# Performance work log

Hardware: AMD Instinct MI355X
Metric: run time of the kernel (lower is better)

Reference implementation:

```python
import jax, jax.numpy as jnp
import numpy as np
import math

N_HEADS = 16

def setup_inputs() -> dict:
    key = jax.random.key(0)
    k1, k2, k3 = jax.random.split(key, 3)
    B, S, D = 2, 2048, 1024
    x = jax.random.normal(k1, (B, S, D), dtype=jnp.float32)
    qkv = 0.01 * jax.random.normal(k2, (3 * D, D), dtype=jnp.float32)
    wo = 0.01 * jax.random.normal(k3, (D, D), dtype=jnp.float32)
    return {"x": x, "qkv": qkv, "wo": wo}

def reference(x, qkv, wo):
    B, S, D = x.shape
    H = N_HEADS
    dh = D // H
    QKV = x @ qkv.T                      # [B,S,3D]
    Q, K, V = jnp.split(QKV, 3, axis=-1)
    q = Q.reshape(B, S, H, dh).transpose(0, 2, 1, 3)  # [B,H,S,dh]
    k = K.reshape(B, S, H, dh).transpose(0, 2, 1, 3)
    v = V.reshape(B, S, H, dh).transpose(0, 2, 1, 3)
    scores = jnp.einsum('bhqd,bhkd->bhqk', q, k) / math.sqrt(float(dh))
    # Faithful to original: multiply by lower-triangular mask, then set
    # exact zeros to -inf (masked positions become 0 then -inf).
    mask = jnp.tril(jnp.ones((S, S), dtype=scores.dtype))
    scores = scores * mask[None, None, :, :]
    scores = jnp.where(scores == 0, -jnp.inf, scores)
    attn = jax.nn.softmax(scores, axis=-1)
    out = jnp.einsum('bhqk,bhkd->bhqd', attn, v)       # [B,H,S,dh]
    out = out.transpose(0, 2, 1, 3).reshape(B, S, D)
    return out @ wo.T
```

## Files before the change

### kernel.cpp

```cpp
#include <hip/hip_runtime.h>

typedef unsigned short u16;
typedef unsigned int u32;
typedef __bf16 bf16x8 __attribute__((ext_vector_type(8)));
typedef float f32x4 __attribute__((ext_vector_type(4)));
typedef u16 u16x4 __attribute__((ext_vector_type(4)));

#define GL2LDS16(g, l)                                                         \
    __builtin_amdgcn_global_load_lds(                                          \
        (__attribute__((address_space(1))) const void*)(g),                    \
        (__attribute__((address_space(3))) void*)(l), 16, 0, 0)

#define SYNC_VM(n) asm volatile("s_waitcnt vmcnt(" #n ")\ns_barrier" ::: "memory")
#define BAR()      asm volatile("s_barrier" ::: "memory")

__device__ __forceinline__ u16 f2bf(float f) {
    union { float f; u32 u; } x; x.f = f;
    u32 r = x.u + 0x7FFFu + ((x.u >> 16) & 1u);
    return (u16)(r >> 16);
}

__device__ __forceinline__ u32 pack2bf(float f0, float f1) {
    union { float f; u32 u; } a, b;
    a.f = f0; b.f = f1;
    return __builtin_amdgcn_perm(b.u + 0x8000u, a.u + 0x8000u, 0x07060302u);
}

__device__ __forceinline__ bf16x8 scale_frag(bf16x8 v) {
#pragma unroll
    for (int i = 0; i < 8; ++i) v[i] = (__bf16)((float)v[i] * 0.1803368801f);
    return v;
}

__global__ __launch_bounds__(256) void convert_all_kernel(const float* __restrict__ x,
                                                          const float* __restrict__ qkv,
                                                          const float* __restrict__ wo,
                                                          u16* __restrict__ out) {
    int i = (blockIdx.x * 256 + threadIdx.x) * 4;
    const float* src;
    int off;
    if (i < 4194304)      { src = x;   off = i; }
    else if (i < 7340032) { src = qkv; off = i - 4194304; }
    else                  { src = wo;  off = i - 7340032; }
    float4 v = *(const float4*)(src + off);
    u16x4 o;
    o.x = f2bf(v.x); o.y = f2bf(v.y); o.z = f2bf(v.z); o.w = f2bf(v.w);
    *(u16x4*)(out + i) = o;
}

template <int TM, bool OUT_BF16>
__global__ __launch_bounds__(256) void gemm_bt(const u16* __restrict__ A,
                                               const u16* __restrict__ B,
                                               void* __restrict__ Cout,
                                               int M, int N, int K) {
    constexpr int MI = TM / 32;
    __shared__ u16 As[2][TM * 32];
    __shared__ u16 Bs[2][128 * 32];
    const int tid = threadIdx.x;
    const int w = tid >> 6, lane = tid & 63, ln = lane & 15, qd = lane >> 4;
    const int wr = w >> 1, wc = w & 1;
    const int m0 = blockIdx.y * TM, n0 = blockIdx.x * 128;

    const int srow = tid >> 2, scol = (tid & 3) * 8;
    const u16* Abase = A + (size_t)(m0 + srow) * K + scol;
    const u16* Bbase = B + (size_t)(n0 + srow) * K + scol;

    f32x4 acc[MI][4] = {};
    const int nsteps = K >> 5;

#pragma unroll
    for (int it = 0; it < TM / 64; ++it)
        GL2LDS16(Abase + (size_t)(it * 64) * K, &As[0][(tid + it * 256) * 8]);
#pragma unroll
    for (int it = 0; it < 2; ++it)
        GL2LDS16(Bbase + (size_t)(it * 64) * K, &Bs[0][(tid + it * 256) * 8]);

    for (int s = 0; s < nsteps; ++s) {
        const u16* Ab = As[s & 1];
        const u16* Bb = Bs[s & 1];
        if (s + 1 < nsteps) {
            const int nk = (s + 1) << 5;
            const int nb = (s + 1) & 1;
#pragma unroll
            for (int it = 0; it < TM / 64; ++it)
                GL2LDS16(Abase + (size_t)(it * 64) * K + nk, &As[nb][(tid + it * 256) * 8]);
#pragma unroll
            for (int it = 0; it < 2; ++it)
                GL2LDS16(Bbase + (size_t)(it * 64) * K + nk, &Bs[nb][(tid + it * 256) * 8]);
            if constexpr (TM == 128) SYNC_VM(4); else SYNC_VM(3);
        } else {
            SYNC_VM(0);
        }

        bf16x8 af[MI], bfr[4];
#pragma unroll
        for (int i = 0; i < MI; ++i)
            af[i] = *(const bf16x8*)&Ab[(wr * (TM / 2) + i * 16 + ln) * 32 + qd * 8];
#pragma unroll
        for (int j = 0; j < 4; ++j)
            bfr[j] = *(const bf16x8*)&Bb[(wc * 64 + j * 16 + ln) * 32 + qd * 8];
#pragma unroll
        for (int i = 0; i < MI; ++i)
#pragma unroll
            for (int j = 0; j < 4; ++j)
                acc[i][j] = __builtin_amdgcn_mfma_f32_16x16x32_bf16(af[i], bfr[j], acc[i][j], 0, 0, 0);
        BAR();
    }

#pragma unroll
    for (int i = 0; i < MI; ++i)
#pragma unroll
        for (int j = 0; j < 4; ++j)
#pragma unroll
            for (int r = 0; r < 4; ++r) {
                int row = m0 + wr * (TM / 2) + i * 16 + qd * 4 + r;
                int col = n0 + wc * 64 + j * 16 + ln;
                float v = acc[i][j][r];
                if constexpr (OUT_BF16)
                    ((u16*)Cout)[(size_t)row * N + col] = f2bf(v);
                else
                    ((float*)Cout)[(size_t)row * N + col] = v;
            }
}

__global__ __launch_bounds__(256) void vtrans_kernel(const u16* __restrict__ QKV,
                                                     u16* __restrict__ VtG) {
    __shared__ u16 T[64 * 72];
    const int tid = threadIdx.x;
    const int bh = blockIdx.y;
    const int b = bh >> 4, h = bh & 15;
    const int s0 = blockIdx.x * 64;
#pragma unroll
    for (int it = 0; it < 2; ++it) {
        int idx = it * 256 + tid;
        int sl = idx >> 3, dg = (idx & 7) << 3;
        union { uint4 v; u16 u[8]; } raw;
        raw.v = *(const uint4*)(QKV + (size_t)(b * 2048 + s0 + sl) * 3072 + 2048 + h * 64 + dg);
#pragma unroll
        for (int j = 0; j < 8; ++j) T[(dg + j) * 72 + sl] = raw.u[j];
    }
    __syncthreads();
#pragma unroll
    for (int it = 0; it < 2; ++it) {
        int idx = it * 256 + tid;
        int d = idx >> 3, sg = (idx & 7) << 3;
        *(uint4*)(VtG + ((size_t)(bh * 64 + d)) * 2048 + s0 + sg) = *(uint4*)&T[d * 72 + sg];
    }
}

__global__ __launch_bounds__(128) void attn_kernel(const u16* __restrict__ QKV,
                                                   const u16* __restrict__ VtG,
                                                   u16* __restrict__ AO) {
    __shared__ u16 Ks[2][64 * 64];
    __shared__ u16 Vts[2][64 * 64];
    __shared__ u16 Pls[2][16 * 64];

    const int tid = threadIdx.x;
    const int w = tid >> 6, lane = tid & 63, ln = lane & 15, qd = lane >> 4;
    const int b = blockIdx.z, h = blockIdx.y;
    const int qtA = blockIdx.x;
    const int qtB = 63 - qtA;
    const int XA = qtA * 32 + w * 16;
    const int XB = qtB * 32 + w * 16;
    const int myqA = XA + ln, myqB = XB + ln;
    const int bh = b * 16 + h;
    const int swz = ln & 7;
    const int nch = (qtB >> 1) + 1;

    const int sr0 = tid >> 3;
    const int sg = (tid & 7) ^ (sr0 & 7);
    const u16* ksrc = QKV + (size_t)(b * 2048 + sr0) * 3072 + 1024 + h * 64 + sg * 8;
    const u16* vsrc = VtG + (size_t)(bh * 64 + sr0) * 2048 + sg * 8;

#pragma unroll
    for (int i = 0; i < 4; ++i) {
        GL2LDS16(ksrc + (size_t)(i * 16) * 3072, &Ks[0][(i * 128 + tid) * 8]);
        GL2LDS16(vsrc + (size_t)(i * 16) * 2048, &Vts[0][(i * 128 + tid) * 8]);
    }

    const u16* qpA = QKV + (size_t)(b * 2048 + myqA) * 3072 + h * 64;
    const u16* qpB = QKV + (size_t)(b * 2048 + myqB) * 3072 + h * 64;
    bf16x8 qfA0 = scale_frag(*(const bf16x8*)(qpA + qd * 8));
    bf16x8 qfA1 = scale_frag(*(const bf16x8*)(qpA + 32 + qd * 8));
    bf16x8 qfB0 = scale_frag(*(const bf16x8*)(qpB + qd * 8));
    bf16x8 qfB1 = scale_frag(*(const bf16x8*)(qpB + 32 + qd * 8));

    f32x4 oA[4] = {}, oB[4] = {};
    float lA = 0.f, lB = 0.f;
    u16* Pw = Pls[w];

    for (int c = 0; c < nch; ++c) {
        if (c + 1 < nch) {
            const int k1 = (c + 1) * 64;
            const int nb = (c + 1) & 1;
#pragma unroll
            for (int i = 0; i < 4; ++i) {
                GL2LDS16(ksrc + (size_t)(k1 + i * 16) * 3072, &Ks[nb][(i * 128 + tid) * 8]);
                GL2LDS16(vsrc + (size_t)(i * 16) * 2048 + k1, &Vts[nb][(i * 128 + tid) * 8]);
            }
            SYNC_VM(8);
        } else {
            SYNC_VM(0);
        }
        const u16* Kb = Ks[c & 1];
        const u16* Vb = Vts[c & 1];
        const bool actA = (c * 64 <= XA + 15);

        f32x4 sA[4], sB[4];
#pragma unroll
        for (int kt = 0; kt < 4; ++kt) {
            const u16* kr = Kb + (kt * 16 + ln) * 64;
            bf16x8 kf0 = *(const bf16x8*)(kr + ((qd ^ swz) * 8));
            bf16x8 kf1 = *(const bf16x8*)(kr + (((qd + 4) ^ swz) * 8));
            f32x4 z = {0.f, 0.f, 0.f, 0.f};
            z = __builtin_amdgcn_mfma_f32_16x16x32_bf16(kf0, qfB0, z, 0, 0, 0);
            z = __builtin_amdgcn_mfma_f32_16x16x32_bf16(kf1, qfB1, z, 0, 0, 0);
            sB[kt] = z;
            if (actA) {
                f32x4 y = {0.f, 0.f, 0.f, 0.f};
                y = __builtin_amdgcn_mfma_f32_16x16x32_bf16(kf0, qfA0, y, 0, 0, 0);
                y = __builtin_amdgcn_mfma_f32_16x16x32_bf16(kf1, qfA1, y, 0, 0, 0);
                sA[kt] = y;
            }
        }

        if (c * 64 + 63 > XB) {
#pragma unroll
            for (int kt = 0; kt < 4; ++kt)
#pragma unroll
                for (int r = 0; r < 4; ++r) {
                    int key = c * 64 + kt * 16 + qd * 4 + r;
                    if (key > myqB) sB[kt][r] = -1e30f;
                }
        }
#pragma unroll
        for (int kt = 0; kt < 4; ++kt) {
            float p0 = exp2f(sB[kt][0]), p1 = exp2f(sB[kt][1]);
            float p2 = exp2f(sB[kt][2]), p3 = exp2f(sB[kt][3]);
            lB += (p0 + p1) + (p2 + p3);
            uint2 pk = {pack2bf(p0, p1), pack2bf(p2, p3)};
            int g = kt * 2 + (qd >> 1);
            *(uint2*)&Pw[ln * 64 + ((g ^ swz) * 8) + (qd & 1) * 4] = pk;
        }
        bf16x8 pfB0 = *(const bf16x8*)&Pw[ln * 64 + ((qd ^ swz) * 8)];
        bf16x8 pfB1 = *(const bf16x8*)&Pw[ln * 64 + (((qd + 4) ^ swz) * 8)];

        bf16x8 pfA0, pfA1;
        if (actA) {
            if (c * 64 + 63 > XA) {
#pragma unroll
                for (int kt = 0; kt < 4; ++kt)
#pragma unroll
                    for (int r = 0; r < 4; ++r) {
                        int key = c * 64 + kt * 16 + qd * 4 + r;
                        if (key > myqA) sA[kt][r] = -1e30f;
                    }
            }
#pragma unroll
            for (int kt = 0; kt < 4; ++kt) {
                float p0 = exp2f(sA[kt][0]), p1 = exp2f(sA[kt][1]);
                float p2 = exp2f(sA[kt][2]), p3 = exp2f(sA[kt][3]);
                lA += (p0 + p1) + (p2 + p3);
                uint2 pk = {pack2bf(p0, p1), pack2bf(p2, p3)};
                int g = kt * 2 + (qd >> 1);
                *(uint2*)&Pw[ln * 64 + ((g ^ swz) * 8) + (qd & 1) * 4] = pk;
            }
            pfA0 = *(const bf16x8*)&Pw[ln * 64 + ((qd ^ swz) * 8)];
            pfA1 = *(const bf16x8*)&Pw[ln * 64 + (((qd + 4) ^ swz) * 8)];
        }

#pragma unroll
        for (int dt = 0; dt < 4; ++dt) {
            const u16* vr = Vb + (dt * 16 + ln) * 64;
            bf16x8 vf0 = *(const bf16x8*)(vr + ((qd ^ swz) * 8));
            bf16x8 vf1 = *(const bf16x8*)(vr + (((qd + 4) ^ swz) * 8));
            oB[dt] = __builtin_amdgcn_mfma_f32_16x16x32_bf16(vf0, pfB0, oB[dt], 0, 0, 0);
            oB[dt] = __builtin_amdgcn_mfma_f32_16x16x32_bf16(vf1, pfB1, oB[dt], 0, 0, 0);
            if (actA) {
                oA[dt] = __builtin_amdgcn_mfma_f32_16x16x32_bf16(vf0, pfA0, oA[dt], 0, 0, 0);
                oA[dt] = __builtin_amdgcn_mfma_f32_16x16x32_bf16(vf1, pfA1, oA[dt], 0, 0, 0);
            }
        }
        BAR();
    }

    lA += __shfl_xor(lA, 16); lA += __shfl_xor(lA, 32);
    lB += __shfl_xor(lB, 16); lB += __shfl_xor(lB, 32);
    float invA = 1.0f / lA, invB = 1.0f / lB;
#pragma unroll
    for (int dt = 0; dt < 4; ++dt) {
        uint2 ovA = {pack2bf(oA[dt][0] * invA, oA[dt][1] * invA),
                     pack2bf(oA[dt][2] * invA, oA[dt][3] * invA)};
        *(uint2*)&AO[(size_t)(b * 2048 + myqA) * 1024 + h * 64 + dt * 16 + qd * 4] = ovA;
        uint2 ovB = {pack2bf(oB[dt][0] * invB, oB[dt][1] * invB),
                     pack2bf(oB[dt][2] * invB, oB[dt][3] * invB)};
        *(uint2*)&AO[(size_t)(b * 2048 + myqB) * 1024 + h * 64 + dt * 16 + qd * 4] = ovB;
    }
}

extern "C" void kernel_launch(void* const* d_in, const int* in_sizes, int n_in,
                              void* d_out, int out_size, void* d_ws, size_t ws_size,
                              hipStream_t stream) {
    const float* x   = (const float*)d_in[0];
    const float* qkv = (const float*)d_in[1];
    const float* wo  = (const float*)d_in[2];
    float* out = (float*)d_out;

    char* ws = (char*)d_ws;
    u16* xb   = (u16*)(ws + 0);
    u16* qkvb = (u16*)(ws + 8388608);
    u16* wob  = (u16*)(ws + 14680064);
    u16* QKVo = (u16*)(ws + 16777216);
    u16* AO   = (u16*)(ws + 41943040);
    u16* VtG  = (u16*)(ws + 0);

    convert_all_kernel<<<8192, 256, 0, stream>>>(x, qkv, wo, xb);

    gemm_bt<128, true><<<dim3(24, 32), 256, 0, stream>>>(xb, qkvb, QKVo, 4096, 3072, 1024);

    vtrans_kernel<<<dim3(32, 32), 256, 0, stream>>>(QKVo, VtG);

    attn_kernel<<<dim3(32, 16, 2), 128, 0, stream>>>(QKVo, VtG, AO);

    gemm_bt<64, false><<<dim3(8, 64), 256, 0, stream>>>(AO, wob, out, 4096, 1024, 1024);
}
```

Before: 202.7 us.

## Split attention key range across two blocks and merge partials in normalize pass

```diff
diff --git a/kernel.cpp b/kernel.cpp
--- a/kernel.cpp
+++ b/kernel.cpp
@@ -24,6 +24,10 @@
     union { float f; u32 u; } a, b;
     a.f = f0; b.f = f1;
     return __builtin_amdgcn_perm(b.u + 0x8000u, a.u + 0x8000u, 0x07060302u);
+}
+
+__device__ __forceinline__ float bits2f(u32 u) {
+    union { u32 u; float f; } x; x.u = u; return x.f;
 }
 
 __device__ __forceinline__ bf16x8 scale_frag(bf16x8 v) {
@@ -148,35 +152,35 @@
     }
 }
 
-__global__ __launch_bounds__(128) void attn_kernel(const u16* __restrict__ QKV,
+__global__ __launch_bounds__(256) void attn_kernel(u16* __restrict__ QKV,
                                                    const u16* __restrict__ VtG,
-                                                   u16* __restrict__ AO) {
+                                                   u16* __restrict__ AO,
+                                                   float* __restrict__ Lp) {
     __shared__ u16 Ks[2][64 * 64];
     __shared__ u16 Vts[2][64 * 64];
-    __shared__ u16 Pls[2][16 * 64];
+    __shared__ u16 Pls[4][16 * 64];
 
     const int tid = threadIdx.x;
     const int w = tid >> 6, lane = tid & 63, ln = lane & 15, qd = lane >> 4;
     const int b = blockIdx.z, h = blockIdx.y;
-    const int qtA = blockIdx.x;
-    const int qtB = 63 - qtA;
-    const int XA = qtA * 32 + w * 16;
-    const int XB = qtB * 32 + w * 16;
+    const int pair = blockIdx.x >> 1;
+    const int k = blockIdx.x & 1;
+    const int qtA = pair, qtB = 31 - pair;
+    const int XA = qtA * 64 + w * 16, XB = qtB * 64 + w * 16;
     const int myqA = XA + ln, myqB = XB + ln;
     const int bh = b * 16 + h;
     const int swz = ln & 7;
-    const int nch = (qtB >> 1) + 1;
+    const int nch = qtB + 1;
 
     const int sr0 = tid >> 3;
     const int sg = (tid & 7) ^ (sr0 & 7);
     const u16* ksrc = QKV + (size_t)(b * 2048 + sr0) * 3072 + 1024 + h * 64 + sg * 8;
     const u16* vsrc = VtG + (size_t)(bh * 64 + sr0) * 2048 + sg * 8;
 
-#pragma unroll
-    for (int i = 0; i < 4; ++i) {
-        GL2LDS16(ksrc + (size_t)(i * 16) * 3072, &Ks[0][(i * 128 + tid) * 8]);
-        GL2LDS16(vsrc + (size_t)(i * 16) * 2048, &Vts[0][(i * 128 + tid) * 8]);
-    }
+    GL2LDS16(ksrc + (size_t)(k * 64) * 3072, &Ks[0][tid * 8]);
+    GL2LDS16(ksrc + (size_t)(k * 64 + 32) * 3072, &Ks[0][tid * 8 + 2048]);
+    GL2LDS16(vsrc + k * 64, &Vts[0][tid * 8]);
+    GL2LDS16(vsrc + k * 64 + 32 * 2048, &Vts[0][tid * 8 + 2048]);
 
     const u16* qpA = QKV + (size_t)(b * 2048 + myqA) * 3072 + h * 64;
     const u16* qpB = QKV + (size_t)(b * 2048 + myqB) * 3072 + h * 64;
@@ -189,21 +193,22 @@
     float lA = 0.f, lB = 0.f;
     u16* Pw = Pls[w];
 
-    for (int c = 0; c < nch; ++c) {
-        if (c + 1 < nch) {
-            const int k1 = (c + 1) * 64;
-            const int nb = (c + 1) & 1;
-#pragma unroll
-            for (int i = 0; i < 4; ++i) {
-                GL2LDS16(ksrc + (size_t)(k1 + i * 16) * 3072, &Ks[nb][(i * 128 + tid) * 8]);
-                GL2LDS16(vsrc + (size_t)(i * 16) * 2048 + k1, &Vts[nb][(i * 128 + tid) * 8]);
-            }
-            SYNC_VM(8);
+    for (int c = k; c < nch; c += 2) {
+        const int j = (c - k) >> 1;
+        const int buf = j & 1;
+        if (c + 2 < nch) {
+            const int k1 = (c + 2) * 64;
+            const int nb = buf ^ 1;
+            GL2LDS16(ksrc + (size_t)k1 * 3072, &Ks[nb][tid * 8]);
+            GL2LDS16(ksrc + (size_t)(k1 + 32) * 3072, &Ks[nb][tid * 8 + 2048]);
+            GL2LDS16(vsrc + k1, &Vts[nb][tid * 8]);
+            GL2LDS16(vsrc + k1 + 32 * 2048, &Vts[nb][tid * 8 + 2048]);
+            SYNC_VM(4);
         } else {
             SYNC_VM(0);
         }
-        const u16* Kb = Ks[c & 1];
-        const u16* Vb = Vts[c & 1];
+        const u16* Kb = Ks[buf];
+        const u16* Vb = Vts[buf];
         const bool actA = (c * 64 <= XA + 15);
 
         f32x4 sA[4], sB[4];
@@ -286,16 +291,44 @@
 
     lA += __shfl_xor(lA, 16); lA += __shfl_xor(lA, 32);
     lB += __shfl_xor(lB, 16); lB += __shfl_xor(lB, 32);
-    float invA = 1.0f / lA, invB = 1.0f / lB;
+    u16* Op = k ? (QKV + 2048) : AO;
+    const size_t ost = k ? 3072 : 1024;
+    if (qd == 0) {
+        Lp[(size_t)k * 65536 + (size_t)(b * 2048 + myqA) * 16 + h] = lA;
+        Lp[(size_t)k * 65536 + (size_t)(b * 2048 + myqB) * 16 + h] = lB;
+    }
 #pragma unroll
     for (int dt = 0; dt < 4; ++dt) {
-        uint2 ovA = {pack2bf(oA[dt][0] * invA, oA[dt][1] * invA),
-                     pack2bf(oA[dt][2] * invA, oA[dt][3] * invA)};
-        *(uint2*)&AO[(size_t)(b * 2048 + myqA) * 1024 + h * 64 + dt * 16 + qd * 4] = ovA;
-        uint2 ovB = {pack2bf(oB[dt][0] * invB, oB[dt][1] * invB),
-                     pack2bf(oB[dt][2] * invB, oB[dt][3] * invB)};
-        *(uint2*)&AO[(size_t)(b * 2048 + myqB) * 1024 + h * 64 + dt * 16 + qd * 4] = ovB;
-    }
+        uint2 ovA = {pack2bf(oA[dt][0], oA[dt][1]), pack2bf(oA[dt][2], oA[dt][3])};
+        *(uint2*)&Op[(size_t)(b * 2048 + myqA) * ost + h * 64 + dt * 16 + qd * 4] = ovA;
+        uint2 ovB = {pack2bf(oB[dt][0], oB[dt][1]), pack2bf(oB[dt][2], oB[dt][3])};
+        *(uint2*)&Op[(size_t)(b * 2048 + myqB) * ost + h * 64 + dt * 16 + qd * 4] = ovB;
+    }
+}
+
+__global__ __launch_bounds__(256) void normalize_kernel(u16* __restrict__ AO,
+                                                        const u16* __restrict__ QKV,
+                                                        const float* __restrict__ Lp) {
+    int g = blockIdx.x * 256 + threadIdx.x;
+    int row = g >> 7;
+    int col = (g & 127) << 3;
+    int h = col >> 6;
+    float l = Lp[(size_t)row * 16 + h] + Lp[65536 + (size_t)row * 16 + h];
+    float inv = 1.0f / l;
+    u16* pa = AO + (size_t)row * 1024 + col;
+    const u16* pb = QKV + (size_t)row * 3072 + 2048 + col;
+    uint4 va = *(uint4*)pa;
+    uint4 vb = *(const uint4*)pb;
+    const u32* a = (const u32*)&va;
+    const u32* bb = (const u32*)&vb;
+    u32 res[4];
+#pragma unroll
+    for (int i = 0; i < 4; ++i) {
+        float a0 = bits2f(a[i] << 16), a1 = bits2f(a[i] & 0xFFFF0000u);
+        float b0 = bits2f(bb[i] << 16), b1 = bits2f(bb[i] & 0xFFFF0000u);
+        res[i] = pack2bf((a0 + b0) * inv, (a1 + b1) * inv);
+    }
+    *(uint4*)pa = *(uint4*)&res[0];
 }
 
 extern "C" void kernel_launch(void* const* d_in, const int* in_sizes, int n_in,
@@ -307,12 +340,13 @@
     float* out = (float*)d_out;
 
     char* ws = (char*)d_ws;
-    u16* xb   = (u16*)(ws + 0);
-    u16* qkvb = (u16*)(ws + 8388608);
-    u16* wob  = (u16*)(ws + 14680064);
-    u16* QKVo = (u16*)(ws + 16777216);
-    u16* AO   = (u16*)(ws + 41943040);
-    u16* VtG  = (u16*)(ws + 0);
+    u16* xb    = (u16*)(ws + 0);
+    u16* qkvb  = (u16*)(ws + 8388608);
+    float* Lp  = (float*)(ws + 8388608);
+    u16* wob   = (u16*)(ws + 14680064);
+    u16* QKVo  = (u16*)(ws + 16777216);
+    u16* AO    = (u16*)(ws + 41943040);
+    u16* VtG   = (u16*)(ws + 0);
 
     convert_all_kernel<<<8192, 256, 0, stream>>>(x, qkv, wo, xb);
 
@@ -320,7 +354,9 @@
 
     vtrans_kernel<<<dim3(32, 32), 256, 0, stream>>>(QKVo, VtG);
 
-    attn_kernel<<<dim3(32, 16, 2), 128, 0, stream>>>(QKVo, VtG, AO);
+    attn_kernel<<<dim3(32, 16, 2), 256, 0, stream>>>(QKVo, VtG, AO, Lp);
+
+    normalize_kernel<<<2048, 256, 0, stream>>>(AO, QKVo, Lp);
 
     gemm_bt<64, false><<<dim3(8, 64), 256, 0, stream>>>(AO, wob, out, 4096, 1024, 1024);
 }
```

Result: no change. 203.3 us (+0.3%).

## Fuse V transpose into QKV GEMM epilogue and widen attention blocks to four waves

Applied to the files above, without the earlier changes.

```diff
diff --git a/kernel.cpp b/kernel.cpp
--- a/kernel.cpp
+++ b/kernel.cpp
@@ -48,10 +48,11 @@
     *(u16x4*)(out + i) = o;
 }
 
-template <int TM, bool OUT_BF16>
+template <int TM, bool OUT_BF16, bool FUSE_VT>
 __global__ __launch_bounds__(256) void gemm_bt(const u16* __restrict__ A,
                                                const u16* __restrict__ B,
                                                void* __restrict__ Cout,
+                                               u16* __restrict__ VtG,
                                                int M, int N, int K) {
     constexpr int MI = TM / 32;
     __shared__ u16 As[2][TM * 32];
@@ -107,6 +108,23 @@
         BAR();
     }
 
+    if (FUSE_VT && n0 >= 2048) {
+        const int bq = m0 >> 11;
+        const int sl = (m0 & 2047) + wr * (TM / 2) + qd * 4;
+#pragma unroll
+        for (int i = 0; i < MI; ++i)
+#pragma unroll
+            for (int j = 0; j < 4; ++j) {
+                int d = n0 - 2048 + wc * 64 + j * 16 + ln;
+                int vrow = (bq * 16 + (d >> 6)) * 64 + (d & 63);
+                u16x4 ov;
+                ov.x = f2bf(acc[i][j][0]); ov.y = f2bf(acc[i][j][1]);
+                ov.z = f2bf(acc[i][j][2]); ov.w = f2bf(acc[i][j][3]);
+                *(u16x4*)&VtG[(size_t)vrow * 2048 + sl + i * 16] = ov;
+            }
+        return;
+    }
+
 #pragma unroll
     for (int i = 0; i < MI; ++i)
 #pragma unroll
@@ -123,60 +141,33 @@
             }
 }
 
-__global__ __launch_bounds__(256) void vtrans_kernel(const u16* __restrict__ QKV,
-                                                     u16* __restrict__ VtG) {
-    __shared__ u16 T[64 * 72];
-    const int tid = threadIdx.x;
-    const int bh = blockIdx.y;
-    const int b = bh >> 4, h = bh & 15;
-    const int s0 = blockIdx.x * 64;
-#pragma unroll
-    for (int it = 0; it < 2; ++it) {
-        int idx = it * 256 + tid;
-        int sl = idx >> 3, dg = (idx & 7) << 3;
-        union { uint4 v; u16 u[8]; } raw;
-        raw.v = *(const uint4*)(QKV + (size_t)(b * 2048 + s0 + sl) * 3072 + 2048 + h * 64 + dg);
-#pragma unroll
-        for (int j = 0; j < 8; ++j) T[(dg + j) * 72 + sl] = raw.u[j];
-    }
-    __syncthreads();
-#pragma unroll
-    for (int it = 0; it < 2; ++it) {
-        int idx = it * 256 + tid;
-        int d = idx >> 3, sg = (idx & 7) << 3;
-        *(uint4*)(VtG + ((size_t)(bh * 64 + d)) * 2048 + s0 + sg) = *(uint4*)&T[d * 72 + sg];
-    }
-}
-
-__global__ __launch_bounds__(128) void attn_kernel(const u16* __restrict__ QKV,
+__global__ __launch_bounds__(256) void attn_kernel(const u16* __restrict__ QKV,
                                                    const u16* __restrict__ VtG,
                                                    u16* __restrict__ AO) {
     __shared__ u16 Ks[2][64 * 64];
     __shared__ u16 Vts[2][64 * 64];
-    __shared__ u16 Pls[2][16 * 64];
+    __shared__ u16 Pls[4][16 * 64];
 
     const int tid = threadIdx.x;
     const int w = tid >> 6, lane = tid & 63, ln = lane & 15, qd = lane >> 4;
     const int b = blockIdx.z, h = blockIdx.y;
     const int qtA = blockIdx.x;
-    const int qtB = 63 - qtA;
-    const int XA = qtA * 32 + w * 16;
-    const int XB = qtB * 32 + w * 16;
+    const int qtB = 31 - qtA;
+    const int XA = qtA * 64 + w * 16, XB = qtB * 64 + w * 16;
     const int myqA = XA + ln, myqB = XB + ln;
     const int bh = b * 16 + h;
     const int swz = ln & 7;
-    const int nch = (qtB >> 1) + 1;
+    const int nch = qtB + 1;
 
     const int sr0 = tid >> 3;
     const int sg = (tid & 7) ^ (sr0 & 7);
     const u16* ksrc = QKV + (size_t)(b * 2048 + sr0) * 3072 + 1024 + h * 64 + sg * 8;
     const u16* vsrc = VtG + (size_t)(bh * 64 + sr0) * 2048 + sg * 8;
 
-#pragma unroll
-    for (int i = 0; i < 4; ++i) {
-        GL2LDS16(ksrc + (size_t)(i * 16) * 3072, &Ks[0][(i * 128 + tid) * 8]);
-        GL2LDS16(vsrc + (size_t)(i * 16) * 2048, &Vts[0][(i * 128 + tid) * 8]);
-    }
+    GL2LDS16(ksrc, &Ks[0][tid * 8]);
+    GL2LDS16(ksrc + (size_t)32 * 3072, &Ks[0][tid * 8 + 2048]);
+    GL2LDS16(vsrc, &Vts[0][tid * 8]);
+    GL2LDS16(vsrc + (size_t)32 * 2048, &Vts[0][tid * 8 + 2048]);
 
     const u16* qpA = QKV + (size_t)(b * 2048 + myqA) * 3072 + h * 64;
     const u16* qpB = QKV + (size_t)(b * 2048 + myqB) * 3072 + h * 64;
@@ -193,18 +184,17 @@
         if (c + 1 < nch) {
             const int k1 = (c + 1) * 64;
             const int nb = (c + 1) & 1;
-#pragma unroll
-            for (int i = 0; i < 4; ++i) {
-                GL2LDS16(ksrc + (size_t)(k1 + i * 16) * 3072, &Ks[nb][(i * 128 + tid) * 8]);
-                GL2LDS16(vsrc + (size_t)(i * 16) * 2048 + k1, &Vts[nb][(i * 128 + tid) * 8]);
-            }
-            SYNC_VM(8);
+            GL2LDS16(ksrc + (size_t)k1 * 3072, &Ks[nb][tid * 8]);
+            GL2LDS16(ksrc + (size_t)(k1 + 32) * 3072, &Ks[nb][tid * 8 + 2048]);
+            GL2LDS16(vsrc + k1, &Vts[nb][tid * 8]);
+            GL2LDS16(vsrc + k1 + 32 * 2048, &Vts[nb][tid * 8 + 2048]);
+            SYNC_VM(4);
         } else {
             SYNC_VM(0);
         }
         const u16* Kb = Ks[c & 1];
         const u16* Vb = Vts[c & 1];
-        const bool actA = (c * 64 <= XA + 15);
+        const bool actA = (c <= qtA);
 
         f32x4 sA[4], sB[4];
 #pragma unroll
@@ -224,7 +214,7 @@
             }
         }
 
-        if (c * 64 + 63 > XB) {
+        if (c == qtB) {
 #pragma unroll
             for (int kt = 0; kt < 4; ++kt)
 #pragma unroll
@@ -247,7 +237,7 @@
 
         bf16x8 pfA0, pfA1;
         if (actA) {
-            if (c * 64 + 63 > XA) {
+            if (c == qtA) {
 #pragma unroll
                 for (int kt = 0; kt < 4; ++kt)
 #pragma unroll
@@ -307,20 +297,20 @@
     float* out = (float*)d_out;
 
     char* ws = (char*)d_ws;
-    u16* xb   = (u16*)(ws + 0);
-    u16* qkvb = (u16*)(ws + 8388608);
-    u16* wob  = (u16*)(ws + 14680064);
-    u16* QKVo = (u16*)(ws + 16777216);
-    u16* AO   = (u16*)(ws + 41943040);
-    u16* VtG  = (u16*)(ws + 0);
+    u16* xb    = (u16*)(ws + 0);
+    u16* qkvb  = (u16*)(ws + 8388608);
+    u16* wob   = (u16*)(ws + 14680064);
+    u16* QKVo  = (u16*)(ws + 16777216);
+    u16* AO    = (u16*)(ws + 41943040);
+    u16* VtG   = (u16*)(ws + 50331648);
 
     convert_all_kernel<<<8192, 256, 0, stream>>>(x, qkv, wo, xb);
 
-    gemm_bt<128, true><<<dim3(24, 32), 256, 0, stream>>>(xb, qkvb, QKVo, 4096, 3072, 1024);
-
-    vtrans_kernel<<<dim3(32, 32), 256, 0, stream>>>(QKVo, VtG);
-
-    attn_kernel<<<dim3(32, 16, 2), 128, 0, stream>>>(QKVo, VtG, AO);
-
-    gemm_bt<64, false><<<dim3(8, 64), 256, 0, stream>>>(AO, wob, out, 4096, 1024, 1024);
-}
+    gemm_bt<128, true, true><<<dim3(24, 32), 256, 0, stream>>>(xb, qkvb, QKVo, VtG,
+                                                               4096, 3072, 1024);
+
+    attn_kernel<<<dim3(16, 16, 2), 256, 0, stream>>>(QKVo, VtG, AO);
+
+    gemm_bt<64, false, false><<<dim3(8, 64), 256, 0, stream>>>(AO, wob, out, nullptr,
+                                                               4096, 1024, 1024);
+}
```

Result: faster. 187.5 us (-7.5%).
